# Kernel optimization log

Measured on AMD Instinct MI355X. Metric: run time of the kernel, lower is better.

The kernel has to match this reference:

```python
import jax, jax.numpy as jnp
import numpy as np

B, T, D = 32, 512, 384
MAX_DUR = 4                 # durations drawn from [0, MAX_DUR]
MAX_FRAMES = T * MAX_DUR    # static padded output length (>= any per-batch total)
PAD_VALUE = 0.0


def setup_inputs() -> dict:
    key = jax.random.key(0)
    k1, k2 = jax.random.split(key)
    xs = jax.random.normal(k1, (B, T, D), dtype=jnp.float32)
    ds = jax.random.randint(k2, (B, T), 0, MAX_DUR + 1).astype(jnp.int64)
    return {"xs": xs, "ds": ds}


def reference(xs, ds):
    # Faithful LengthRegulator.forward with alpha == 1.0 (default):
    # expand each phoneme embedding by its duration, pad sequences to a
    # common length with pad_value. Instead of a per-sample Python loop +
    # repeat_interleave, we compute cumulative durations and map every
    # output frame t to its source phoneme via searchsorted (gather).
    ds = ds.astype(jnp.int32)
    # ESPnet safeguard: rows with all-zero durations are filled with 1s.
    row_all_zero = (ds.sum(axis=1) == 0)[:, None]          # (B, 1)
    ds = jnp.where(row_all_zero, 1, ds)

    cum = jnp.cumsum(ds, axis=1)                            # (B, T)
    totals = cum[:, -1]                                     # (B,)
    t = jnp.arange(MAX_FRAMES, dtype=jnp.int32)             # (MAX_FRAMES,)
    # frame t belongs to phoneme i where cum[i-1] <= t < cum[i]
    idx = jax.vmap(lambda c: jnp.searchsorted(c, t, side='right'))(cum)  # (B, MAX_FRAMES)
    idx = jnp.clip(idx, 0, T - 1)
    valid = t[None, :] < totals[:, None]                    # (B, MAX_FRAMES)

    out = jnp.take_along_axis(xs, idx[:, :, None], axis=1)  # (B, MAX_FRAMES, D)
    return jnp.where(valid[:, :, None], out, jnp.asarray(PAD_VALUE, xs.dtype))
```

## Files before the change

kernel.cpp:

```cpp
#include <hip/hip_runtime.h>

#define NB 32
#define NT 512
#define NC 96
#define NFRAMES 2048
#define SLICES 16
#define FPS (NFRAMES / SLICES)
#define ITERS (FPS * NC / NT)

__global__ __launch_bounds__(NT) void lr_fused_kernel(const int* __restrict__ ds,
                                                      const float4* __restrict__ xs,
                                                      float4* __restrict__ out) {
    __shared__ int cum[NT];
    __shared__ int sidx[FPS];
    const int t = threadIdx.x;
    const int slice = blockIdx.x;
    const int b = blockIdx.y;

    cum[t] = ds[b * NT + t];
    __syncthreads();
    #pragma unroll
    for (int off = 1; off < NT; off <<= 1) {
        int v = (t >= off) ? cum[t - off] : 0;
        __syncthreads();
        cum[t] += v;
        __syncthreads();
    }

    int total = cum[NT - 1];
    if (total == 0) {
        cum[t] = t + 1;
        total = NT;
    }
    __syncthreads();

    if (t < FPS) {
        const int p = slice * FPS + t;
        int j = -1;
        if (p < total) {
            int lo = 0, hi = NT;
            while (lo < hi) {
                const int mid = (lo + hi) >> 1;
                if (cum[mid] > p) hi = mid; else lo = mid + 1;
            }
            j = lo;
        }
        sidx[t] = j;
    }
    __syncthreads();

    const float4* __restrict__ xrow = xs + (size_t)b * NT * NC;
    float4* __restrict__ orow = out + ((size_t)b * NFRAMES + (size_t)slice * FPS) * NC;
    const float4 z = make_float4(0.f, 0.f, 0.f, 0.f);
    #pragma unroll
    for (int it = 0; it < ITERS; ++it) {
        const int e = it * NT + t;
        const int fr = e / NC;
        const int c = e - fr * NC;
        const int j = sidx[fr];
        orow[e] = (j >= 0) ? xrow[j * NC + c] : z;
    }
}

extern "C" void kernel_launch(void* const* d_in, const int* in_sizes, int n_in,
                              void* d_out, int out_size, void* d_ws, size_t ws_size,
                              hipStream_t stream) {
    const float* xs = (const float*)d_in[0];
    const int*   ds = (const int*)d_in[1];
    float* out = (float*)d_out;
    (void)in_sizes; (void)n_in; (void)out_size; (void)d_ws; (void)ws_size;

    dim3 grid(SLICES, NB);
    lr_fused_kernel<<<grid, NT, 0, stream>>>(ds, (const float4*)xs, (float4*)out);
}
```

Measured before the change: 132.1 us.

## Use wave-shuffle scan, batched unconditional gathers, and nontemporal output stores

Replaces the shared-memory Hillis-Steele prefix sum, which needed many block-wide barriers, with a wave-level shuffle scan followed by a small cross-wave combine. The copy loop now issues 8 gathers back to back, loading row 0 for padding frames instead of branching, so more loads are in flight at once. Output is written with nontemporal stores to avoid polluting the cache. The trade-offs are extra reads for padded frames and higher register pressure from the batched loads.

```diff
diff --git a/kernel.cpp b/kernel.cpp
--- a/kernel.cpp
+++ b/kernel.cpp
@@ -7,30 +7,43 @@
 #define SLICES 16
 #define FPS (NFRAMES / SLICES)
 #define ITERS (FPS * NC / NT)
+#define NWAVES (NT / 64)
+
+typedef float f4 __attribute__((ext_vector_type(4)));
 
 __global__ __launch_bounds__(NT) void lr_fused_kernel(const int* __restrict__ ds,
-                                                      const float4* __restrict__ xs,
-                                                      float4* __restrict__ out) {
+                                                      const f4* __restrict__ xs,
+                                                      f4* __restrict__ out) {
     __shared__ int cum[NT];
+    __shared__ int wsum[NWAVES];
     __shared__ int sidx[FPS];
     const int t = threadIdx.x;
+    const int lane = t & 63;
+    const int w = t >> 6;
     const int slice = blockIdx.x;
     const int b = blockIdx.y;
 
-    cum[t] = ds[b * NT + t];
+    int s = ds[b * NT + t];
+    #pragma unroll
+    for (int off = 1; off < 64; off <<= 1) {
+        int u = __shfl_up(s, off);
+        if (lane >= off) s += u;
+    }
+    if (lane == 63) wsum[w] = s;
     __syncthreads();
+    int woff = 0, tot = 0;
     #pragma unroll
-    for (int off = 1; off < NT; off <<= 1) {
-        int v = (t >= off) ? cum[t - off] : 0;
-        __syncthreads();
-        cum[t] += v;
-        __syncthreads();
+    for (int i = 0; i < NWAVES; ++i) {
+        const int v = wsum[i];
+        woff += (i < w) ? v : 0;
+        tot += v;
     }
-
-    int total = cum[NT - 1];
+    int total = tot;
     if (total == 0) {
         cum[t] = t + 1;
         total = NT;
+    } else {
+        cum[t] = s + woff;
     }
     __syncthreads();
 
@@ -49,16 +62,28 @@
     }
     __syncthreads();
 
-    const float4* __restrict__ xrow = xs + (size_t)b * NT * NC;
-    float4* __restrict__ orow = out + ((size_t)b * NFRAMES + (size_t)slice * FPS) * NC;
-    const float4 z = make_float4(0.f, 0.f, 0.f, 0.f);
+    const f4* __restrict__ xrow = xs + (size_t)b * NT * NC;
+    f4* __restrict__ orow = out + ((size_t)b * NFRAMES + (size_t)slice * FPS) * NC;
     #pragma unroll
-    for (int it = 0; it < ITERS; ++it) {
-        const int e = it * NT + t;
-        const int fr = e / NC;
-        const int c = e - fr * NC;
-        const int j = sidx[fr];
-        orow[e] = (j >= 0) ? xrow[j * NC + c] : z;
+    for (int g = 0; g < ITERS / 8; ++g) {
+        f4 v[8];
+        int neg[8];
+        #pragma unroll
+        for (int u = 0; u < 8; ++u) {
+            const int e = (g * 8 + u) * NT + t;
+            const int fr = e / NC;
+            const int c = e - fr * NC;
+            const int j = sidx[fr];
+            neg[u] = (j < 0);
+            const int jj = (j < 0) ? 0 : j;
+            v[u] = xrow[jj * NC + c];
+        }
+        #pragma unroll
+        for (int u = 0; u < 8; ++u) {
+            const int e = (g * 8 + u) * NT + t;
+            f4 r = neg[u] ? (f4)(0.f) : v[u];
+            __builtin_nontemporal_store(r, &orow[e]);
+        }
     }
 }
 
@@ -71,5 +96,5 @@
     (void)in_sizes; (void)n_in; (void)out_size; (void)d_ws; (void)ws_size;
 
     dim3 grid(SLICES, NB);
-    lr_fused_kernel<<<grid, NT, 0, stream>>>(ds, (const float4*)xs, (float4*)out);
+    lr_fused_kernel<<<grid, NT, 0, stream>>>(ds, (const f4*)xs, (f4*)out);
 }
```

Measured after the change: 134.3 us. Within noise of the previous version (+1.7%).
